# Kernel optimization log

Hardware: AMD Instinct MI355X
Metric: run time of the kernel (lower is better)

## Reference

```python
import jax, jax.numpy as jnp
import numpy as np

D_MODEL, D_K, D_V, H = 1024, 64, 64, 16
B, NQ, NK = 4, 1024, 1024


def setup_inputs() -> dict:
    key = jax.random.key(0)
    ks = jax.random.split(key, 16)
    xav = lambda k, shape: jax.random.uniform(k, shape, jnp.float32, -1.0, 1.0) * np.sqrt(6.0 / (shape[0] + shape[1])).astype(np.float32)
    return {
        "queries": jax.random.normal(ks[0], (B, NQ, D_MODEL), jnp.float32),
        "keys": jax.random.normal(ks[1], (B, NK, D_MODEL), jnp.float32),
        "values": jax.random.normal(ks[2], (B, NK, D_MODEL), jnp.float32),
        "attention_weights": jax.random.uniform(ks[3], (B, H, NQ, NK), jnp.float32),
        "attention_mask": jax.random.randint(ks[4], (B, H, NQ, NK), 0, 2, jnp.int32),
        "Wq": xav(ks[5], (H * D_K, D_MODEL)), "bq": jnp.zeros((H * D_K,), jnp.float32),
        "Wk": xav(ks[6], (H * D_K, D_MODEL)), "bk": jnp.zeros((H * D_K,), jnp.float32),
        "Wv": xav(ks[7], (H * D_V, D_MODEL)), "bv": jnp.zeros((H * D_V,), jnp.float32),
        "Wo": xav(ks[8], (D_MODEL, H * D_V)), "bo": jnp.zeros((D_MODEL,), jnp.float32),
    }


def reference(queries, keys, values, attention_weights, attention_mask,
              Wq, bq, Wk, bk, Wv, bv, Wo, bo):
    b, nq, _ = queries.shape
    nk = keys.shape[1]
    # projections, split heads: (b, h, n, d)
    q = (queries @ Wq.T + bq).reshape(b, nq, H, D_K).transpose(0, 2, 1, 3)
    k = (keys @ Wk.T + bk).reshape(b, nk, H, D_K).transpose(0, 2, 1, 3)
    v = (values @ Wv.T + bv).reshape(b, nk, H, D_V).transpose(0, 2, 1, 3)
    scale = jnp.asarray(1.0 / np.sqrt(D_K), q.dtype)
    att = jnp.einsum('bhqd,bhkd->bhqk', q, k) * scale
    att_map = att  # returned pre-bias/mask scores, as in the torch code (att.clone())
    # way='mul', use_knn=False path
    att = att * attention_weights
    att = jnp.where(attention_mask == 0, -jnp.inf, att)
    att = jax.nn.softmax(att, axis=-1)
    out = jnp.einsum('bhqk,bhkd->bqhd', att, v).reshape(b, nq, H * D_V)
    out = out @ Wo.T + bo
    return out, att_map
```

## Files before the change

kernel.cpp:

```cpp
#include <hip/hip_runtime.h>
#include <stdint.h>
#include <math.h>

#define B_ 4
#define H_ 16
#define DM_ 1024
#define NQ_ 1024
#define NK_ 1024

typedef __attribute__((ext_vector_type(4))) float f32x4;
typedef __attribute__((ext_vector_type(4))) short s16x4;
typedef __attribute__((ext_vector_type(8))) short s16x8;

#define MFMA(a, b, c) __builtin_amdgcn_mfma_f32_16x16x32_bf16(a, b, c, 0, 0, 0)

static __device__ __forceinline__ short f2bf(float f) {
  union { float f; uint32_t u; } v; v.f = f;
  uint32_t r = (v.u + 0x7FFFu + ((v.u >> 16) & 1u)) >> 16;
  return (short)(uint16_t)r;
}

static __device__ __forceinline__ float bf2f(short s) {
  union { uint32_t u; float f; } v;
  v.u = ((uint32_t)(uint16_t)s) << 16;
  return v.f;
}

static __device__ __forceinline__ void gload_lds16(const void* g, void* s) {
  __builtin_amdgcn_global_load_lds(
      (const __attribute__((address_space(1))) uint32_t*)g,
      (__attribute__((address_space(3))) uint32_t*)s, 16, 0, 0);
}

__global__ void k_cvt(const float* __restrict__ src, short* __restrict__ dst, int n) {
  int i = (blockIdx.x * 256 + threadIdx.x) * 4;
  if (i + 3 < n) {
    f32x4 v = *(const f32x4*)(src + i);
    s16x4 o;
    o.x = f2bf(v.x); o.y = f2bf(v.y); o.z = f2bf(v.z); o.w = f2bf(v.w);
    *(s16x4*)(dst + i) = o;
  }
}

__global__ __launch_bounds__(256, 2) void k_gemm(
    const short* __restrict__ A, const short* __restrict__ Bw,
    const float* __restrict__ bias, void* __restrict__ outp, int mode) {
  __shared__ short As[128 * 64];
  __shared__ short Bs[128 * 64];
  const int tid = threadIdx.x;
  const int w = tid >> 6, l = tid & 63;
  const int wm = w >> 1, wn = w & 1;
  const int lr = l & 15, lg = l >> 4;
  const int m0 = blockIdx.x * 128, n0 = blockIdx.y * 128;

  f32x4 acc[4][4] = {};

  for (int kt = 0; kt < 16; ++kt) {
    __syncthreads();
#pragma unroll
    for (int q = 0; q < 4; ++q) {
      const int slot = (w * 4 + q) * 64 + l;
      const int row = slot >> 3;
      const int chunk = (slot & 7) ^ (row & 7);
      const size_t goff = (size_t)row * 1024 + (size_t)kt * 64 + chunk * 8;
      gload_lds16(A + (size_t)m0 * 1024 + goff, (char*)As + (w * 4 + q) * 1024);
      gload_lds16(Bw + (size_t)n0 * 1024 + goff, (char*)Bs + (w * 4 + q) * 1024);
    }
    asm volatile("s_waitcnt vmcnt(0)");
    __syncthreads();
#pragma unroll
    for (int ks = 0; ks < 2; ++ks) {
      s16x8 af[4], bfr[4];
#pragma unroll
      for (int mi = 0; mi < 4; ++mi) {
        const int row = wm * 64 + mi * 16 + lr;
        const int chunk = (ks * 4 + lg) ^ (row & 7);
        af[mi] = *(const s16x8*)(As + row * 64 + chunk * 8);
      }
#pragma unroll
      for (int ni = 0; ni < 4; ++ni) {
        const int row = wn * 64 + ni * 16 + lr;
        const int chunk = (ks * 4 + lg) ^ (row & 7);
        bfr[ni] = *(const s16x8*)(Bs + row * 64 + chunk * 8);
      }
#pragma unroll
      for (int mi = 0; mi < 4; ++mi)
#pragma unroll
        for (int ni = 0; ni < 4; ++ni)
          acc[mi][ni] = MFMA(af[mi], bfr[ni], acc[mi][ni]);
    }
  }

#pragma unroll
  for (int mi = 0; mi < 4; ++mi) {
#pragma unroll
    for (int ni = 0; ni < 4; ++ni) {
      const int gm0 = m0 + wm * 64 + mi * 16 + lg * 4;
      const int gc = n0 + wn * 64 + ni * 16 + lr;
      const float bv = bias[gc];
      if (mode == 2) {
        float* o = (float*)outp;
#pragma unroll
        for (int r = 0; r < 4; ++r)
          o[(size_t)(gm0 + r) * 1024 + gc] = acc[mi][ni][r] + bv;
      } else if (mode == 0) {
        short* o = (short*)outp;
        const int h = gc >> 6, d = gc & 63;
#pragma unroll
        for (int r = 0; r < 4; ++r) {
          const int gm = gm0 + r;
          const int b = gm >> 10, np = gm & 1023;
          o[((size_t)(b * 16 + h) * 1024 + np) * 64 + d] = f2bf(acc[mi][ni][r] + bv);
        }
      } else {
        short* o = (short*)outp;
        const int h = gc >> 6, d = gc & 63;
        const int b = gm0 >> 10, np0 = gm0 & 1023;
        s16x4 pk;
        pk.x = f2bf(acc[mi][ni][0] + bv);
        pk.y = f2bf(acc[mi][ni][1] + bv);
        pk.z = f2bf(acc[mi][ni][2] + bv);
        pk.w = f2bf(acc[mi][ni][3] + bv);
        *(s16x4*)(o + ((size_t)(b * 16 + h) * 64 + d) * 1024 + np0) = pk;
      }
    }
  }
}

__global__ __launch_bounds__(256, 4) void k_attn(
    const short* __restrict__ qws, const short* __restrict__ kws,
    const short* __restrict__ vtws,
    const float* __restrict__ attw, const int* __restrict__ attm,
    float* __restrict__ att_map, short* __restrict__ o_part,
    float* __restrict__ mpart, float* __restrict__ lpart) {
  __shared__ short p_lds[4 * 16 * 64];
  const int tid = threadIdx.x;
  const int w = tid >> 6, l = tid & 63;
  const int lr = l & 15, lg = l >> 4;
  const int bh = blockIdx.y;
  const int split = blockIdx.z;
  const int q0 = blockIdx.x * 64 + w * 16;
  char* const pl = (char*)p_lds + w * 2048;

  const short* qb = qws + ((size_t)bh * NQ_ + q0 + lr) * 64 + lg * 8;
  const s16x8 qf0 = *(const s16x8*)(qb);
  const s16x8 qf1 = *(const s16x8*)(qb + 32);

  f32x4 o[4] = {};
  float mrow[4], lrow[4];
#pragma unroll
  for (int r = 0; r < 4; ++r) { mrow[r] = -3.0e38f; lrow[r] = 0.0f; }

  const size_t mapRowBase = ((size_t)bh * NQ_ + q0 + lg * 4) * (size_t)NK_ + lr;

  for (int kt = split * 8; kt < split * 8 + 8; ++kt) {
    f32x4 s[4];
    const short* kb0 = kws + ((size_t)bh * NK_ + kt * 64 + lr) * 64 + lg * 8;
#pragma unroll
    for (int fn = 0; fn < 4; ++fn) {
      const short* kb = kb0 + fn * (16 * 64);
      const s16x8 kf0 = *(const s16x8*)(kb);
      const s16x8 kf1 = *(const s16x8*)(kb + 32);
      f32x4 z = {};
      z = MFMA(qf0, kf0, z);
      z = MFMA(qf1, kf1, z);
      s[fn] = z;
    }
    float p[4][4];
    const size_t base = mapRowBase + (size_t)kt * 64;
#pragma unroll
    for (int fn = 0; fn < 4; ++fn) {
#pragma unroll
      for (int r = 0; r < 4; ++r) {
        const size_t idx = base + (size_t)r * NK_ + fn * 16;
        const float sv = s[fn][r] * 0.125f;
        att_map[idx] = sv;
        const float wv = attw[idx];
        const int mv = attm[idx];
        p[fn][r] = mv ? sv * wv : -1.0e30f;
      }
    }
#pragma unroll
    for (int r = 0; r < 4; ++r) {
      float t = fmaxf(fmaxf(p[0][r], p[1][r]), fmaxf(p[2][r], p[3][r]));
      t = fmaxf(t, __shfl_xor(t, 1, 64));
      t = fmaxf(t, __shfl_xor(t, 2, 64));
      t = fmaxf(t, __shfl_xor(t, 4, 64));
      t = fmaxf(t, __shfl_xor(t, 8, 64));
      const float mn = fmaxf(mrow[r], t);
      const float corr = __expf(mrow[r] - mn);
      mrow[r] = mn;
      lrow[r] *= corr;
      o[0][r] *= corr; o[1][r] *= corr; o[2][r] *= corr; o[3][r] *= corr;
      float rs = 0.0f;
#pragma unroll
      for (int fn = 0; fn < 4; ++fn) {
        const float e = __expf(p[fn][r] - mn);
        p[fn][r] = e;
        rs += e;
      }
      rs += __shfl_xor(rs, 1, 64);
      rs += __shfl_xor(rs, 2, 64);
      rs += __shfl_xor(rs, 4, 64);
      rs += __shfl_xor(rs, 8, 64);
      lrow[r] += rs;
    }
#pragma unroll
    for (int fn = 0; fn < 4; ++fn) {
#pragma unroll
      for (int r = 0; r < 4; ++r) {
        const int row = lg * 4 + r;
        const int col = fn * 16 + lr;
        const int chunk = (col >> 3) ^ (row & 7);
        *(short*)(pl + row * 128 + chunk * 16 + (col & 7) * 2) = f2bf(p[fn][r]);
      }
    }
    asm volatile("s_waitcnt lgkmcnt(0)" ::: "memory");
    __builtin_amdgcn_sched_barrier(0);
    const short* vb0 = vtws + ((size_t)bh * 64 + lr) * (size_t)NK_ + (size_t)kt * 64 + lg * 8;
#pragma unroll
    for (int ks = 0; ks < 2; ++ks) {
      const int chunk = (ks * 4 + lg) ^ (lr & 7);
      const s16x8 pa = *(const s16x8*)(pl + lr * 128 + chunk * 16);
#pragma unroll
      for (int g = 0; g < 4; ++g) {
        const s16x8 vf = *(const s16x8*)(vb0 + (size_t)g * 16 * NK_ + ks * 32);
        o[g] = MFMA(pa, vf, o[g]);
      }
    }
  }

  short* op = o_part + (size_t)split * 4194304;
  const int qrow_base = bh * NQ_ + q0 + lg * 4;
#pragma unroll
  for (int r = 0; r < 4; ++r) {
    const size_t orow = (size_t)(qrow_base + r) * 64 + lr;
#pragma unroll
    for (int g = 0; g < 4; ++g)
      op[orow + g * 16] = f2bf(o[g][r]);
    if (lr == 0) {
      mpart[split * 65536 + qrow_base + r] = mrow[r];
      lpart[split * 65536 + qrow_base + r] = lrow[r];
    }
  }
}

__global__ __launch_bounds__(256, 4) void k_merge(
    const short* __restrict__ o_part, const float* __restrict__ mpart,
    const float* __restrict__ lpart, short* __restrict__ aout) {
  const int t = blockIdx.x * 256 + threadIdx.x;
  const int row = t >> 4;
  const int d0 = (t & 15) * 4;
  const float m1 = mpart[row], m2 = mpart[65536 + row];
  const float l1 = lpart[row], l2 = lpart[65536 + row];
  const float M = fmaxf(m1, m2);
  const float c1 = __expf(m1 - M), c2 = __expf(m2 - M);
  const float inv = 1.0f / (l1 * c1 + l2 * c2);
  const s16x4 a = *(const s16x4*)(o_part + (size_t)row * 64 + d0);
  const s16x4 b = *(const s16x4*)(o_part + 4194304 + (size_t)row * 64 + d0);
  const int bh = row >> 10, q = row & 1023;
  const int bb = bh >> 4, h = bh & 15;
  s16x4 o;
#pragma unroll
  for (int j = 0; j < 4; ++j)
    o[j] = f2bf((bf2f(a[j]) * c1 + bf2f(b[j]) * c2) * inv);
  *(s16x4*)(aout + ((size_t)(bb * 1024 + q) * 1024 + h * 64 + d0)) = o;
}

extern "C" void kernel_launch(void* const* d_in, const int* in_sizes, int n_in,
                              void* d_out, int out_size, void* d_ws, size_t ws_size,
                              hipStream_t stream) {
  const float* queries = (const float*)d_in[0];
  const float* keys    = (const float*)d_in[1];
  const float* values  = (const float*)d_in[2];
  const float* attw    = (const float*)d_in[3];
  const int*   attm    = (const int*)d_in[4];
  const float* Wq = (const float*)d_in[5];
  const float* bq = (const float*)d_in[6];
  const float* Wk = (const float*)d_in[7];
  const float* bk = (const float*)d_in[8];
  const float* Wv = (const float*)d_in[9];
  const float* bv = (const float*)d_in[10];
  const float* Wo = (const float*)d_in[11];
  const float* bo = (const float*)d_in[12];

  float* out = (float*)d_out;
  float* att_map = out + (size_t)B_ * NQ_ * DM_;

  short* ws  = (short*)d_ws;
  short* WqB = ws;
  short* WkB = WqB + 1048576;
  short* WvB = WkB + 1048576;
  short* WoB = WvB + 1048576;
  short* Xq  = WoB + 1048576;
  short* Xk  = Xq + 4194304;
  short* Xv  = Xk + 4194304;
  short* qws = Xv + 4194304;
  short* kws = qws + 4194304;
  short* vtw = kws + 4194304;
  short* aout = vtw + 4194304;

  short* o_part = Xq;
  float* mpart  = (float*)Xv;
  float* lpart  = mpart + 131072;

  k_cvt<<<4096, 256, 0, stream>>>(queries, Xq, 4194304);
  k_cvt<<<4096, 256, 0, stream>>>(keys, Xk, 4194304);
  k_cvt<<<4096, 256, 0, stream>>>(values, Xv, 4194304);
  k_cvt<<<1024, 256, 0, stream>>>(Wq, WqB, 1048576);
  k_cvt<<<1024, 256, 0, stream>>>(Wk, WkB, 1048576);
  k_cvt<<<1024, 256, 0, stream>>>(Wv, WvB, 1048576);
  k_cvt<<<1024, 256, 0, stream>>>(Wo, WoB, 1048576);

  dim3 gg(32, 8);
  k_gemm<<<gg, 256, 0, stream>>>(Xq, WqB, bq, qws, 0);
  k_gemm<<<gg, 256, 0, stream>>>(Xk, WkB, bk, kws, 0);
  k_gemm<<<gg, 256, 0, stream>>>(Xv, WvB, bv, vtw, 1);

  dim3 ga(16, 64, 2);
  k_attn<<<ga, 256, 0, stream>>>(qws, kws, vtw, attw, attm, att_map,
                                 o_part, mpart, lpart);
  k_merge<<<4096, 256, 0, stream>>>(o_part, mpart, lpart, aout);

  k_gemm<<<gg, 256, 0, stream>>>(aout, WoB, bo, out, 2);
}
```

Measured before the change: 371.0 us.

## Transpose QK^T MFMA output so each lane holds contiguous key columns for vector I/O

Swaps the MFMA operand order so the score fragment is transposed: each lane now owns one query row and four consecutive key columns. The att_map stores and the attention-weight and mask loads become 16-byte vector accesses instead of scalar strided ones. Softmax row statistics become one value per lane, reduced across lane groups, and the correction factor is shuffled back to the O accumulator layout. P is written to LDS as packed 4-element vectors. The cost being targeted is the large number of uncoalesced scalar global accesses to the B*H*NQ*NK tensors, at the price of extra cross-lane shuffles for the correction factors.

```diff
diff --git a/kernel.cpp b/kernel.cpp
--- a/kernel.cpp
+++ b/kernel.cpp
@@ -9,6 +9,7 @@
 #define NK_ 1024
 
 typedef __attribute__((ext_vector_type(4))) float f32x4;
+typedef __attribute__((ext_vector_type(4))) int   s32x4;
 typedef __attribute__((ext_vector_type(4))) short s16x4;
 typedef __attribute__((ext_vector_type(8))) short s16x8;
 
@@ -147,11 +148,9 @@
   const s16x8 qf1 = *(const s16x8*)(qb + 32);
 
   f32x4 o[4] = {};
-  float mrow[4], lrow[4];
-#pragma unroll
-  for (int r = 0; r < 4; ++r) { mrow[r] = -3.0e38f; lrow[r] = 0.0f; }
-
-  const size_t mapRowBase = ((size_t)bh * NQ_ + q0 + lg * 4) * (size_t)NK_ + lr;
+  float mrow = -3.0e38f, lrow = 0.0f;
+
+  const size_t rowBase = ((size_t)bh * NQ_ + q0 + lr) * (size_t)NK_;
 
   for (int kt = split * 8; kt < split * 8 + 8; ++kt) {
     f32x4 s[4];
@@ -162,58 +161,59 @@
       const s16x8 kf0 = *(const s16x8*)(kb);
       const s16x8 kf1 = *(const s16x8*)(kb + 32);
       f32x4 z = {};
-      z = MFMA(qf0, kf0, z);
-      z = MFMA(qf1, kf1, z);
+      z = MFMA(kf0, qf0, z);
+      z = MFMA(kf1, qf1, z);
       s[fn] = z;
     }
     float p[4][4];
-    const size_t base = mapRowBase + (size_t)kt * 64;
+    const size_t tbase = rowBase + (size_t)kt * 64 + lg * 4;
 #pragma unroll
     for (int fn = 0; fn < 4; ++fn) {
+      const size_t idx = tbase + fn * 16;
+      f32x4 sv;
+#pragma unroll
+      for (int r = 0; r < 4; ++r) sv[r] = s[fn][r] * 0.125f;
+      *(f32x4*)(att_map + idx) = sv;
+      const f32x4 wv = *(const f32x4*)(attw + idx);
+      const s32x4 mv = *(const s32x4*)(attm + idx);
+#pragma unroll
+      for (int r = 0; r < 4; ++r)
+        p[fn][r] = mv[r] ? sv[r] * wv[r] : -1.0e30f;
+    }
+    float t = -3.0e38f;
+#pragma unroll
+    for (int fn = 0; fn < 4; ++fn)
+#pragma unroll
+      for (int r = 0; r < 4; ++r) t = fmaxf(t, p[fn][r]);
+    t = fmaxf(t, __shfl_xor(t, 16, 64));
+    t = fmaxf(t, __shfl_xor(t, 32, 64));
+    const float mn = fmaxf(mrow, t);
+    const float corr = __expf(mrow - mn);
+    mrow = mn;
+    float rs = 0.0f;
+#pragma unroll
+    for (int fn = 0; fn < 4; ++fn)
 #pragma unroll
       for (int r = 0; r < 4; ++r) {
-        const size_t idx = base + (size_t)r * NK_ + fn * 16;
-        const float sv = s[fn][r] * 0.125f;
-        att_map[idx] = sv;
-        const float wv = attw[idx];
-        const int mv = attm[idx];
-        p[fn][r] = mv ? sv * wv : -1.0e30f;
-      }
-    }
-#pragma unroll
-    for (int r = 0; r < 4; ++r) {
-      float t = fmaxf(fmaxf(p[0][r], p[1][r]), fmaxf(p[2][r], p[3][r]));
-      t = fmaxf(t, __shfl_xor(t, 1, 64));
-      t = fmaxf(t, __shfl_xor(t, 2, 64));
-      t = fmaxf(t, __shfl_xor(t, 4, 64));
-      t = fmaxf(t, __shfl_xor(t, 8, 64));
-      const float mn = fmaxf(mrow[r], t);
-      const float corr = __expf(mrow[r] - mn);
-      mrow[r] = mn;
-      lrow[r] *= corr;
-      o[0][r] *= corr; o[1][r] *= corr; o[2][r] *= corr; o[3][r] *= corr;
-      float rs = 0.0f;
-#pragma unroll
-      for (int fn = 0; fn < 4; ++fn) {
         const float e = __expf(p[fn][r] - mn);
         p[fn][r] = e;
         rs += e;
       }
-      rs += __shfl_xor(rs, 1, 64);
-      rs += __shfl_xor(rs, 2, 64);
-      rs += __shfl_xor(rs, 4, 64);
-      rs += __shfl_xor(rs, 8, 64);
-      lrow[r] += rs;
+    rs += __shfl_xor(rs, 16, 64);
+    rs += __shfl_xor(rs, 32, 64);
+    lrow = lrow * corr + rs;
+#pragma unroll
+    for (int r = 0; r < 4; ++r) {
+      const float cr = __shfl(corr, lg * 4 + r, 64);
+      o[0][r] *= cr; o[1][r] *= cr; o[2][r] *= cr; o[3][r] *= cr;
     }
 #pragma unroll
     for (int fn = 0; fn < 4; ++fn) {
-#pragma unroll
-      for (int r = 0; r < 4; ++r) {
-        const int row = lg * 4 + r;
-        const int col = fn * 16 + lr;
-        const int chunk = (col >> 3) ^ (row & 7);
-        *(short*)(pl + row * 128 + chunk * 16 + (col & 7) * 2) = f2bf(p[fn][r]);
-      }
+      s16x4 pk;
+      pk.x = f2bf(p[fn][0]); pk.y = f2bf(p[fn][1]);
+      pk.z = f2bf(p[fn][2]); pk.w = f2bf(p[fn][3]);
+      const int chunk = (fn * 2 + (lg >> 1)) ^ (lr & 7);
+      *(s16x4*)(pl + lr * 128 + chunk * 16 + (lg & 1) * 8) = pk;
     }
     asm volatile("s_waitcnt lgkmcnt(0)" ::: "memory");
     __builtin_amdgcn_sched_barrier(0);
@@ -238,10 +238,10 @@
 #pragma unroll
     for (int g = 0; g < 4; ++g)
       op[orow + g * 16] = f2bf(o[g][r]);
-    if (lr == 0) {
-      mpart[split * 65536 + qrow_base + r] = mrow[r];
-      lpart[split * 65536 + qrow_base + r] = lrow[r];
-    }
+  }
+  if (l < 16) {
+    mpart[split * 65536 + bh * NQ_ + q0 + l] = mrow;
+    lpart[split * 65536 + bh * NQ_ + q0 + l] = lrow;
   }
 }
 
```

Result: slower. 390.1 us (+5.1%).

## Transpose score tiles through LDS for vectorized row-contiguous mask/weight access

Applied to the files above, without the earlier changes.

Computes S^T via swapped MFMA operands, stages the score tile in swizzled LDS, and re-reads it so each lane owns 4 contiguous key columns of one query row. This lets attention_weights, attention_mask and att_map use 16-byte vector loads and stores instead of scattered scalar accesses, and the softmax correction factors are passed back to the MFMA row layout through a small LDS array. It adds an LDS round-trip and more shared memory per block, and lowers the occupancy hint from 4 to 3 blocks.

```diff
diff --git a/kernel.cpp b/kernel.cpp
--- a/kernel.cpp
+++ b/kernel.cpp
@@ -9,6 +9,7 @@
 #define NK_ 1024
 
 typedef __attribute__((ext_vector_type(4))) float f32x4;
+typedef __attribute__((ext_vector_type(4))) int   s32x4;
 typedef __attribute__((ext_vector_type(4))) short s16x4;
 typedef __attribute__((ext_vector_type(8))) short s16x8;
 
@@ -127,101 +128,107 @@
   }
 }
 
-__global__ __launch_bounds__(256, 4) void k_attn(
+__global__ __launch_bounds__(256, 3) void k_attn(
     const short* __restrict__ qws, const short* __restrict__ kws,
     const short* __restrict__ vtws,
     const float* __restrict__ attw, const int* __restrict__ attm,
     float* __restrict__ att_map, short* __restrict__ o_part,
     float* __restrict__ mpart, float* __restrict__ lpart) {
+  __shared__ f32x4 s_lds[4 * 256];
   __shared__ short p_lds[4 * 16 * 64];
+  __shared__ float st_lds[4 * 16];
   const int tid = threadIdx.x;
   const int w = tid >> 6, l = tid & 63;
   const int lr = l & 15, lg = l >> 4;
   const int bh = blockIdx.y;
   const int split = blockIdx.z;
   const int q0 = blockIdx.x * 64 + w * 16;
-  char* const pl = (char*)p_lds + w * 2048;
+  f32x4* const sw = s_lds + w * 256;
+  char* const pw = (char*)p_lds + w * 2048;
+  float* const stw = st_lds + w * 16;
 
   const short* qb = qws + ((size_t)bh * NQ_ + q0 + lr) * 64 + lg * 8;
   const s16x8 qf0 = *(const s16x8*)(qb);
   const s16x8 qf1 = *(const s16x8*)(qb + 32);
 
   f32x4 o[4] = {};
-  float mrow[4], lrow[4];
-#pragma unroll
-  for (int r = 0; r < 4; ++r) { mrow[r] = -3.0e38f; lrow[r] = 0.0f; }
-
-  const size_t mapRowBase = ((size_t)bh * NQ_ + q0 + lg * 4) * (size_t)NK_ + lr;
+  float m4[4], l4[4];
+#pragma unroll
+  for (int it = 0; it < 4; ++it) { m4[it] = -3.0e38f; l4[it] = 0.0f; }
+
+  const size_t linBase = ((size_t)bh * NQ_ + q0 + lg) * (size_t)NK_ + lr * 4;
 
   for (int kt = split * 8; kt < split * 8 + 8; ++kt) {
     f32x4 s[4];
     const short* kb0 = kws + ((size_t)bh * NK_ + kt * 64 + lr) * 64 + lg * 8;
 #pragma unroll
     for (int fn = 0; fn < 4; ++fn) {
-      const short* kb = kb0 + fn * (16 * 64);
-      const s16x8 kf0 = *(const s16x8*)(kb);
-      const s16x8 kf1 = *(const s16x8*)(kb + 32);
+      const short* kb = kb0 + fn * 1024;
       f32x4 z = {};
-      z = MFMA(qf0, kf0, z);
-      z = MFMA(qf1, kf1, z);
+      z = MFMA(*(const s16x8*)kb, qf0, z);
+      z = MFMA(*(const s16x8*)(kb + 32), qf1, z);
       s[fn] = z;
     }
-    float p[4][4];
-    const size_t base = mapRowBase + (size_t)kt * 64;
-#pragma unroll
-    for (int fn = 0; fn < 4; ++fn) {
-#pragma unroll
-      for (int r = 0; r < 4; ++r) {
-        const size_t idx = base + (size_t)r * NK_ + fn * 16;
-        const float sv = s[fn][r] * 0.125f;
-        att_map[idx] = sv;
-        const float wv = attw[idx];
-        const int mv = attm[idx];
-        p[fn][r] = mv ? sv * wv : -1.0e30f;
-      }
-    }
-#pragma unroll
-    for (int r = 0; r < 4; ++r) {
-      float t = fmaxf(fmaxf(p[0][r], p[1][r]), fmaxf(p[2][r], p[3][r]));
+#pragma unroll
+    for (int fn = 0; fn < 4; ++fn)
+      sw[lr * 16 + ((fn * 4 + lg) ^ lr)] = s[fn];
+    asm volatile("s_waitcnt lgkmcnt(0)" ::: "memory");
+    __builtin_amdgcn_sched_barrier(0);
+    f32x4 sv4[4], wv4[4];
+    s32x4 mv4[4];
+#pragma unroll
+    for (int it = 0; it < 4; ++it) {
+      const int q = it * 4 + lg;
+      sv4[it] = sw[q * 16 + (lr ^ q)];
+      const size_t ga = linBase + (size_t)(it * 4) * NK_ + kt * 64;
+      wv4[it] = *(const f32x4*)(attw + ga);
+      mv4[it] = *(const s32x4*)(attm + ga);
+    }
+#pragma unroll
+    for (int it = 0; it < 4; ++it) {
+      const int q = it * 4 + lg;
+      f32x4 sv;
+#pragma unroll
+      for (int j = 0; j < 4; ++j) sv[j] = sv4[it][j] * 0.125f;
+      const size_t ga = linBase + (size_t)(it * 4) * NK_ + kt * 64;
+      *(f32x4*)(att_map + ga) = sv;
+      float p[4];
+#pragma unroll
+      for (int j = 0; j < 4; ++j)
+        p[j] = mv4[it][j] ? sv[j] * wv4[it][j] : -1.0e30f;
+      float t = fmaxf(fmaxf(p[0], p[1]), fmaxf(p[2], p[3]));
       t = fmaxf(t, __shfl_xor(t, 1, 64));
       t = fmaxf(t, __shfl_xor(t, 2, 64));
       t = fmaxf(t, __shfl_xor(t, 4, 64));
       t = fmaxf(t, __shfl_xor(t, 8, 64));
-      const float mn = fmaxf(mrow[r], t);
-      const float corr = __expf(mrow[r] - mn);
-      mrow[r] = mn;
-      lrow[r] *= corr;
-      o[0][r] *= corr; o[1][r] *= corr; o[2][r] *= corr; o[3][r] *= corr;
+      const float mn = fmaxf(m4[it], t);
+      const float corr = __expf(m4[it] - mn);
+      m4[it] = mn;
       float rs = 0.0f;
 #pragma unroll
-      for (int fn = 0; fn < 4; ++fn) {
-        const float e = __expf(p[fn][r] - mn);
-        p[fn][r] = e;
-        rs += e;
-      }
+      for (int j = 0; j < 4; ++j) { p[j] = __expf(p[j] - mn); rs += p[j]; }
       rs += __shfl_xor(rs, 1, 64);
       rs += __shfl_xor(rs, 2, 64);
       rs += __shfl_xor(rs, 4, 64);
       rs += __shfl_xor(rs, 8, 64);
-      lrow[r] += rs;
-    }
-#pragma unroll
-    for (int fn = 0; fn < 4; ++fn) {
-#pragma unroll
-      for (int r = 0; r < 4; ++r) {
-        const int row = lg * 4 + r;
-        const int col = fn * 16 + lr;
-        const int chunk = (col >> 3) ^ (row & 7);
-        *(short*)(pl + row * 128 + chunk * 16 + (col & 7) * 2) = f2bf(p[fn][r]);
-      }
+      l4[it] = l4[it] * corr + rs;
+      s16x4 pk;
+      pk.x = f2bf(p[0]); pk.y = f2bf(p[1]); pk.z = f2bf(p[2]); pk.w = f2bf(p[3]);
+      *(s16x4*)(pw + q * 128 + (((lr >> 1) ^ (q & 7)) << 4) + (lr & 1) * 8) = pk;
+      if (lr == 0) stw[q] = corr;
     }
     asm volatile("s_waitcnt lgkmcnt(0)" ::: "memory");
     __builtin_amdgcn_sched_barrier(0);
+#pragma unroll
+    for (int r = 0; r < 4; ++r) {
+      const float cr = stw[lg * 4 + r];
+      o[0][r] *= cr; o[1][r] *= cr; o[2][r] *= cr; o[3][r] *= cr;
+    }
     const short* vb0 = vtws + ((size_t)bh * 64 + lr) * (size_t)NK_ + (size_t)kt * 64 + lg * 8;
 #pragma unroll
     for (int ks = 0; ks < 2; ++ks) {
       const int chunk = (ks * 4 + lg) ^ (lr & 7);
-      const s16x8 pa = *(const s16x8*)(pl + lr * 128 + chunk * 16);
+      const s16x8 pa = *(const s16x8*)(pw + lr * 128 + chunk * 16);
 #pragma unroll
       for (int g = 0; g < 4; ++g) {
         const s16x8 vf = *(const s16x8*)(vb0 + (size_t)g * 16 * NK_ + ks * 32);
@@ -238,9 +245,13 @@
 #pragma unroll
     for (int g = 0; g < 4; ++g)
       op[orow + g * 16] = f2bf(o[g][r]);
-    if (lr == 0) {
-      mpart[split * 65536 + qrow_base + r] = mrow[r];
-      lpart[split * 65536 + qrow_base + r] = lrow[r];
+  }
+  if (lr == 0) {
+#pragma unroll
+    for (int it = 0; it < 4; ++it) {
+      const int qrow = bh * NQ_ + q0 + it * 4 + lg;
+      mpart[split * 65536 + qrow] = m4[it];
+      lpart[split * 65536 + qrow] = l4[it];
     }
   }
 }
```

After: 377.1 us. No clear change (+1.6%).
